# Optimization experiments

Measured on AMD Instinct MI355X. Metric: run time of the kernel, lower is better.

## Reference

```python
import jax, jax.numpy as jnp
import numpy as np

WS = 7  # local window size
NH = 12  # num heads


def _ln(x, g, b, eps=1e-5):
    m = x.mean(-1, keepdims=True)
    v = ((x - m) ** 2).mean(-1, keepdims=True)
    return (x - m) / jnp.sqrt(v + eps) * g + b


def setup_inputs() -> dict:
    key = jax.random.key(0)
    ks = jax.random.split(key, 10)
    B, C, H, W = 8, 384, 112, 112
    r = 4
    s = lambda k, sh: jax.random.normal(k, sh, jnp.float32) * 0.02
    return {
        "x": jax.random.normal(ks[0], (B, C, H, W), jnp.float32),
        "w_qkv": s(ks[1], (3 * C, C)),
        "b_qkv": s(ks[2], (3 * C,)),
        "w_o": s(ks[3], (C, C)),
        "b_o": s(ks[4], (C,)),
        "w_c1": s(ks[5], (C // r, C)),
        "b_c1": s(ks[6], (C // r,)),
        "w_c2": s(ks[7], (C, C // r)),
        "b_c2": s(ks[8], (C,)),
        "g1": jnp.ones((C,), jnp.float32),
        "be1": jnp.zeros((C,), jnp.float32),
        "g2": jnp.ones((C,), jnp.float32),
        "be2": jnp.zeros((C,), jnp.float32),
    }


def reference(x, w_qkv, b_qkv, w_o, b_o, w_c1, b_c1, w_c2, b_c2, g1, be1, g2, be2):
    B, C, H, W = x.shape
    hd = C // NH
    Hw, Ww = H // WS, W // WS
    # window partition: [B,C,H,W] -> [B*Hw*Ww, WS*WS, C]
    win = x.reshape(B, C, Hw, WS, Ww, WS).transpose(0, 2, 4, 1, 3, 5)
    win = win.reshape(-1, C, WS * WS).transpose(0, 2, 1)
    Bn, T, _ = win.shape
    # torch MultiheadAttention: packed in_proj, scaled dot-product, out_proj
    qkv = win @ w_qkv.T + b_qkv
    q, k, v = jnp.split(qkv, 3, axis=-1)
    q = q.reshape(Bn, T, NH, hd)
    k = k.reshape(Bn, T, NH, hd)
    v = v.reshape(Bn, T, NH, hd)
    scores = jnp.einsum('bqhd,bkhd->bhqk', q, k) / jnp.sqrt(jnp.float32(hd))
    a = jax.nn.softmax(scores, axis=-1)
    o = jnp.einsum('bhqk,bkhd->bqhd', a, v).reshape(Bn, T, C)
    o = o @ w_o.T + b_o
    # window reverse: [Bn, WS*WS, C] -> [B,C,H,W]
    attn_out = o.reshape(B, Hw, Ww, WS, WS, C).transpose(0, 5, 1, 3, 2, 4).reshape(B, C, H, W)
    x = x + attn_out
    x = _ln(x.transpose(0, 2, 3, 1), g1, be1).transpose(0, 3, 1, 2)
    # 1x1 conv -> Mish -> 1x1 conv
    h = jnp.einsum('bchw,oc->bohw', x, w_c1) + b_c1[None, :, None, None]
    h = h * jnp.tanh(jax.nn.softplus(h))
    h = jnp.einsum('bchw,oc->bohw', h, w_c2) + b_c2[None, :, None, None]
    x = x + h
    x = _ln(x.transpose(0, 2, 3, 1), g2, be2).transpose(0, 3, 1, 2)
    return x
```

## Files before the change

kernel.cpp:

```cpp
#include <hip/hip_runtime.h>

typedef unsigned short u16;
typedef unsigned int u32;
typedef __bf16 bf16x8 __attribute__((ext_vector_type(8)));
typedef float f32x4 __attribute__((ext_vector_type(4)));

#define NPIX 100352
#define CDIM 384

static __device__ __forceinline__ u16 f2bf(float f) {
  union { float f; u32 u; } un; un.f = f;
  u32 u = un.u;
  return (u16)((u + 0x7fffu + ((u >> 16) & 1u)) >> 16);
}

static __device__ __forceinline__ f32x4 mfma_bf16(bf16x8 a, bf16x8 b, f32x4 c) {
  return __builtin_amdgcn_mfma_f32_16x16x32_bf16(a, b, c, 0, 0, 0);
}

__global__ __launch_bounds__(256) void k_pad_bf16(const float* __restrict__ src,
                                                  u16* __restrict__ dst,
                                                  int R, int Csrc, int Rp, int Cp) {
  int idx = blockIdx.x * 256 + threadIdx.x;
  if (idx >= Rp * Cp) return;
  int r = idx / Cp, c = idx - r * Cp;
  float v = (r < R && c < Csrc) ? src[r * Csrc + c] : 0.f;
  dst[idx] = f2bf(v);
}

__global__ __launch_bounds__(256) void k_gather(const float* __restrict__ x,
                                                float* __restrict__ xw_f32,
                                                u16* __restrict__ xw_bf16) {
  int bid = blockIdx.x;
  int cg = bid % 6;
  int tmp = bid / 6;
  int hh = tmp % 112;
  int b = tmp / 112;
  __shared__ float tile[64][113];
  int tid = threadIdx.x;
  const float* src = x + (((size_t)b * 384 + cg * 64) * 112 + hh) * 112;
  for (int idx = tid; idx < 64 * 112; idx += 256) {
    int c = idx / 112, w = idx - c * 112;
    tile[c][w] = src[(size_t)c * 12544 + w];
  }
  __syncthreads();
  int wh = hh / 7, i = hh - wh * 7;
  for (int idx = tid; idx < 64 * 112; idx += 256) {
    int w = idx >> 6, c = idx & 63;
    int ww = w / 7, j = w - ww * 7;
    size_t t = (((size_t)b * 16 + wh) * 16 + ww) * 49 + i * 7 + j;
    float v = tile[c][w];
    size_t o = t * 384 + cg * 64 + c;
    xw_f32[o] = v;
    xw_bf16[o] = f2bf(v);
  }
}

__global__ __launch_bounds__(256) void k_scatter(const float* __restrict__ t_in,
                                                 float* __restrict__ out) {
  int bid = blockIdx.x;
  int cg = bid % 6;
  int tmp = bid / 6;
  int hh = tmp % 112;
  int b = tmp / 112;
  __shared__ float tile[64][113];
  int tid = threadIdx.x;
  int wh = hh / 7, i = hh - wh * 7;
  for (int idx = tid; idx < 64 * 112; idx += 256) {
    int w = idx >> 6, c = idx & 63;
    int ww = w / 7, j = w - ww * 7;
    size_t t = (((size_t)b * 16 + wh) * 16 + ww) * 49 + i * 7 + j;
    tile[c][w] = t_in[t * 384 + cg * 64 + c];
  }
  __syncthreads();
  float* dst = out + (((size_t)b * 384 + cg * 64) * 112 + hh) * 112;
  for (int idx = tid; idx < 64 * 112; idx += 256) {
    int c = idx / 112, w = idx - c * 112;
    dst[(size_t)c * 12544 + w] = tile[c][w];
  }
}

template <int OUT_BF16, int MISH>
__global__ __launch_bounds__(256) void k_gemm(const u16* __restrict__ A,
                                              const u16* __restrict__ B,
                                              const float* __restrict__ bias, int bias_n,
                                              void* __restrict__ C, int K, int ldc) {
  __shared__ u16 lA[128 * 64];
  __shared__ u16 lB[128 * 64];
  int tid = threadIdx.x;
  int m0 = blockIdx.x * 128;
  int n0 = blockIdx.y * 128;
  int wave = tid >> 6, lane = tid & 63;
  int wr = wave >> 1, wc = wave & 1;
  int lr = lane & 15, lk = (lane >> 4) << 3;
  f32x4 acc[4][4] = {};
  int kt_n = K >> 6;
  for (int kt = 0; kt < kt_n; ++kt) {
    int k0 = kt << 6;
#pragma unroll
    for (int i = 0; i < 4; ++i) {
      int chunk = i * 256 + tid;
      int row = chunk >> 3, c8 = (chunk & 7) << 3;
      *(uint4*)(&lA[(row << 6) + c8]) = *(const uint4*)(A + (size_t)(m0 + row) * K + k0 + c8);
      *(uint4*)(&lB[(row << 6) + c8]) = *(const uint4*)(B + (size_t)(n0 + row) * K + k0 + c8);
    }
    __syncthreads();
#pragma unroll
    for (int ks = 0; ks < 2; ++ks) {
      bf16x8 af[4], bf[4];
#pragma unroll
      for (int f = 0; f < 4; ++f) {
        af[f] = *(const bf16x8*)(&lA[((wr * 64 + f * 16 + lr) << 6) + ks * 32 + lk]);
        bf[f] = *(const bf16x8*)(&lB[((wc * 64 + f * 16 + lr) << 6) + ks * 32 + lk]);
      }
#pragma unroll
      for (int fm = 0; fm < 4; ++fm)
#pragma unroll
        for (int fn = 0; fn < 4; ++fn)
          acc[fm][fn] = mfma_bf16(af[fm], bf[fn], acc[fm][fn]);
    }
    __syncthreads();
  }
  int lg = lane >> 4;
#pragma unroll
  for (int fm = 0; fm < 4; ++fm)
#pragma unroll
    for (int fn = 0; fn < 4; ++fn) {
      int col = n0 + wc * 64 + fn * 16 + lr;
      float bi = (col < bias_n) ? bias[col] : 0.f;
#pragma unroll
      for (int r = 0; r < 4; ++r) {
        int row = m0 + wr * 64 + fm * 16 + lg * 4 + r;
        float v = acc[fm][fn][r] + bi;
        if (MISH) {
          float sp = (v > 20.f) ? v : log1pf(__expf(v));
          v = v * tanhf(sp);
        }
        if (OUT_BF16)
          ((u16*)C)[(size_t)row * ldc + col] = f2bf(v);
        else
          ((float*)C)[(size_t)row * ldc + col] = v;
      }
    }
}

__global__ __launch_bounds__(256) void k_attn(const u16* __restrict__ qkv,
                                              u16* __restrict__ o) {
  __shared__ u16 VT[4][32 * 64];
  __shared__ u16 P[4][64 * 64];
  int tid = threadIdx.x, wave = tid >> 6, lane = tid & 63;
  int gid = blockIdx.x * 4 + wave;
  int win = gid / 12, head = gid - win * 12;
  size_t tb = (size_t)win * 49;
  const u16* q_base = qkv + tb * 1152 + head * 32;
  const u16* k_base = q_base + 384;
  const u16* v_base = q_base + 768;
  u16* vt = VT[wave];
  u16* pp = P[wave];
  int lr = lane & 15, lg = lane >> 4, lk = lg << 3;

  {
    int tok = lane;
    if (tok < 49) {
      const u32* vr = (const u32*)(v_base + (size_t)tok * 1152);
#pragma unroll
      for (int q8 = 0; q8 < 4; ++q8) {
        uint4 a = *(const uint4*)(vr + q8 * 4);
        u32 arr[4] = {a.x, a.y, a.z, a.w};
#pragma unroll
        for (int p = 0; p < 4; ++p) {
          int d = q8 * 8 + p * 2;
          vt[d * 64 + tok] = (u16)(arr[p] & 0xffffu);
          vt[(d + 1) * 64 + tok] = (u16)(arr[p] >> 16);
        }
      }
    } else {
#pragma unroll
      for (int d = 0; d < 32; ++d) vt[d * 64 + tok] = 0;
    }
  }

  f32x4 sc[4][4] = {};
  {
    bf16x8 qf[4], kf[4];
#pragma unroll
    for (int f = 0; f < 4; ++f) {
      int tq = f * 16 + lr; if (tq > 48) tq = 48;
      qf[f] = *(const bf16x8*)(q_base + (size_t)tq * 1152 + lk);
      kf[f] = *(const bf16x8*)(k_base + (size_t)tq * 1152 + lk);
    }
#pragma unroll
    for (int fm = 0; fm < 4; ++fm)
#pragma unroll
      for (int fn = 0; fn < 4; ++fn)
        sc[fm][fn] = mfma_bf16(qf[fm], kf[fn], sc[fm][fn]);
  }

  const float scale = 0.17677669529663687f;
  float denom[4][4];
#pragma unroll
  for (int fm = 0; fm < 4; ++fm)
#pragma unroll
    for (int r = 0; r < 4; ++r) {
      float mx = -1e30f;
#pragma unroll
      for (int fn = 0; fn < 4; ++fn) {
        int col = fn * 16 + lr;
        float s = sc[fm][fn][r] * scale;
        if (col >= 49) s = -1e30f;
        sc[fm][fn][r] = s;
        mx = fmaxf(mx, s);
      }
      for (int off = 8; off; off >>= 1) mx = fmaxf(mx, __shfl_xor(mx, off));
      float sum = 0.f;
#pragma unroll
      for (int fn = 0; fn < 4; ++fn) {
        float e = __expf(sc[fm][fn][r] - mx);
        sc[fm][fn][r] = e;
        sum += e;
      }
      for (int off = 8; off; off >>= 1) sum += __shfl_xor(sum, off);
      denom[fm][r] = sum;
    }

#pragma unroll
  for (int fm = 0; fm < 4; ++fm)
#pragma unroll
    for (int fn = 0; fn < 4; ++fn) {
      int col = fn * 16 + lr;
#pragma unroll
      for (int r = 0; r < 4; ++r) {
        int row = fm * 16 + lg * 4 + r;
        pp[row * 64 + col] = f2bf(sc[fm][fn][r]);
      }
    }
  __syncthreads();

  f32x4 oa[4][2] = {};
#pragma unroll
  for (int ks = 0; ks < 2; ++ks) {
    bf16x8 pf[4], vf[2];
#pragma unroll
    for (int f = 0; f < 4; ++f)
      pf[f] = *(const bf16x8*)(&pp[(f * 16 + lr) * 64 + ks * 32 + lk]);
#pragma unroll
    for (int f = 0; f < 2; ++f)
      vf[f] = *(const bf16x8*)(&vt[(f * 16 + lr) * 64 + ks * 32 + lk]);
#pragma unroll
    for (int fm = 0; fm < 4; ++fm)
#pragma unroll
      for (int fn = 0; fn < 2; ++fn)
        oa[fm][fn] = mfma_bf16(pf[fm], vf[fn], oa[fm][fn]);
  }

#pragma unroll
  for (int fm = 0; fm < 4; ++fm)
#pragma unroll
    for (int fn = 0; fn < 2; ++fn)
#pragma unroll
      for (int r = 0; r < 4; ++r) {
        int q = fm * 16 + lg * 4 + r;
        if (q < 49) {
          float v = oa[fm][fn][r] / denom[fm][r];
          int d = fn * 16 + lr;
          o[(tb + q) * 384 + head * 32 + d] = f2bf(v);
        }
      }
}

template <int WRITE_BF16>
__global__ __launch_bounds__(256) void k_ln(const float* __restrict__ a,
                                            const float* __restrict__ bres,
                                            const float* __restrict__ g,
                                            const float* __restrict__ be,
                                            float* __restrict__ yf,
                                            u16* __restrict__ yb) {
  int wave = threadIdx.x >> 6, lane = threadIdx.x & 63;
  size_t t = (size_t)blockIdx.x * 4 + wave;
  const float* ar = a + t * 384;
  const float* br = bres + t * 384;
  float v[6];
  float s = 0.f, s2 = 0.f;
#pragma unroll
  for (int p = 0; p < 3; ++p) {
    int idx = p * 128 + lane * 2;
    float2 x1 = *(const float2*)(ar + idx);
    float2 x2 = *(const float2*)(br + idx);
    float a0 = x1.x + x2.x, a1 = x1.y + x2.y;
    v[p * 2] = a0; v[p * 2 + 1] = a1;
    s += a0 + a1; s2 += a0 * a0 + a1 * a1;
  }
  for (int off = 32; off; off >>= 1) {
    s += __shfl_xor(s, off);
    s2 += __shfl_xor(s2, off);
  }
  float mean = s * (1.f / 384.f);
  float var = s2 * (1.f / 384.f) - mean * mean;
  float rs = rsqrtf(var + 1e-5f);
  float* yr = yf + t * 384;
#pragma unroll
  for (int p = 0; p < 3; ++p) {
    int idx = p * 128 + lane * 2;
    float2 gg = *(const float2*)(g + idx);
    float2 bb = *(const float2*)(be + idx);
    float y0 = (v[p * 2] - mean) * rs * gg.x + bb.x;
    float y1 = (v[p * 2 + 1] - mean) * rs * gg.y + bb.y;
    *(float2*)(yr + idx) = make_float2(y0, y1);
    if (WRITE_BF16) {
      u32 pk = (u32)f2bf(y0) | ((u32)f2bf(y1) << 16);
      *(u32*)(yb + t * 384 + idx) = pk;
    }
  }
}

extern "C" void kernel_launch(void* const* d_in, const int* in_sizes, int n_in,
                              void* d_out, int out_size, void* d_ws, size_t ws_size,
                              hipStream_t stream) {
  const float* x     = (const float*)d_in[0];
  const float* w_qkv = (const float*)d_in[1];
  const float* b_qkv = (const float*)d_in[2];
  const float* w_o   = (const float*)d_in[3];
  const float* b_o   = (const float*)d_in[4];
  const float* w_c1  = (const float*)d_in[5];
  const float* b_c1  = (const float*)d_in[6];
  const float* w_c2  = (const float*)d_in[7];
  const float* b_c2  = (const float*)d_in[8];
  const float* g1    = (const float*)d_in[9];
  const float* be1   = (const float*)d_in[10];
  const float* g2    = (const float*)d_in[11];
  const float* be2   = (const float*)d_in[12];

  char* ws = (char*)d_ws;
  float* xw_f32 = (float*)ws;
  u16* xw_bf16 = (u16*)(ws + 154140672);
  char* reg3 = ws + 231211008;
  u16* qkv = (u16*)reg3;
  float* attn = (float*)reg3;
  u16* h1 = (u16*)reg3;
  float* hbuf = (float*)(reg3 + 25690112);
  u16* wq_b  = (u16*)(ws + 462422016);
  u16* wo_b  = (u16*)(ws + 463306752);
  u16* wc1_b = (u16*)(ws + 463601664);
  u16* wc2_b = (u16*)(ws + 463699968);
  u16* o_b = xw_bf16;
  u16* y_b = xw_bf16;

  k_pad_bf16<<<1728, 256, 0, stream>>>(w_qkv, wq_b, 1152, 384, 1152, 384);
  k_pad_bf16<<<576, 256, 0, stream>>>(w_o, wo_b, 384, 384, 384, 384);
  k_pad_bf16<<<192, 256, 0, stream>>>(w_c1, wc1_b, 96, 384, 128, 384);
  k_pad_bf16<<<192, 256, 0, stream>>>(w_c2, wc2_b, 384, 96, 384, 128);

  k_gather<<<5376, 256, 0, stream>>>(x, xw_f32, xw_bf16);

  k_gemm<1, 0><<<dim3(784, 9), 256, 0, stream>>>(xw_bf16, wq_b, b_qkv, 1152, (void*)qkv, 384, 1152);

  k_attn<<<6144, 256, 0, stream>>>(qkv, o_b);

  k_gemm<0, 0><<<dim3(784, 3), 256, 0, stream>>>(o_b, wo_b, b_o, 384, (void*)attn, 384, 384);

  k_ln<1><<<25088, 256, 0, stream>>>(xw_f32, attn, g1, be1, xw_f32, y_b);

  k_gemm<1, 1><<<dim3(784, 1), 256, 0, stream>>>(y_b, wc1_b, b_c1, 96, (void*)h1, 384, 128);

  k_gemm<0, 0><<<dim3(784, 3), 256, 0, stream>>>(h1, wc2_b, b_c2, 384, (void*)hbuf, 128, 384);

  k_ln<0><<<25088, 256, 0, stream>>>(xw_f32, hbuf, g2, be2, xw_f32, (u16*)nullptr);

  k_scatter<<<5376, 256, 0, stream>>>(xw_f32, (float*)d_out);
}
```

Measured before the change: 1.096 ms.

## Use direct global-to-LDS loads with XOR swizzle and XCD-aware tile remap in GEMM

The GEMM tile loads now go straight from global memory into LDS through global_load_lds, so the data no longer passes through registers, and the LDS layout uses an XOR swizzle to avoid bank conflicts on fragment reads. Workgroup IDs are remapped so that consecutive tiles land on the same XCD, and the grid axes are swapped so the N tiles of one M row share cached A data. The swizzle has to be consistent between the write and read sides. Synchronisation is unchanged, with no double buffering.

```diff
diff --git a/kernel.cpp b/kernel.cpp
--- a/kernel.cpp
+++ b/kernel.cpp
@@ -16,6 +16,11 @@
 
 static __device__ __forceinline__ f32x4 mfma_bf16(bf16x8 a, bf16x8 b, f32x4 c) {
   return __builtin_amdgcn_mfma_f32_16x16x32_bf16(a, b, c, 0, 0, 0);
+}
+
+static __device__ __forceinline__ void gload_lds16(const u16* g, u16* l) {
+  __builtin_amdgcn_global_load_lds((const __attribute__((address_space(1))) void*)g,
+                                   (__attribute__((address_space(3))) void*)l, 16, 0, 0);
 }
 
 __global__ __launch_bounds__(256) void k_pad_bf16(const float* __restrict__ src,
@@ -88,30 +93,39 @@
   __shared__ u16 lA[128 * 64];
   __shared__ u16 lB[128 * 64];
   int tid = threadIdx.x;
-  int m0 = blockIdx.x * 128;
-  int n0 = blockIdx.y * 128;
+  int nbn = gridDim.x;
+  int nwg = nbn * gridDim.y;
+  int id = blockIdx.y * nbn + blockIdx.x;
+  int q = nwg >> 3;
+  int id2 = (id & 7) * q + (id >> 3);
+  int n0 = (id2 % nbn) * 128;
+  int m0 = (id2 / nbn) * 128;
   int wave = tid >> 6, lane = tid & 63;
   int wr = wave >> 1, wc = wave & 1;
-  int lr = lane & 15, lk = (lane >> 4) << 3;
+  int lr = lane & 15, lg = lane >> 4;
+  int lrow = lane >> 3, lchunk = lane & 7;
+  int csw = (lchunk ^ lrow) << 3;
+  int rsw = lr & 7;
   f32x4 acc[4][4] = {};
   int kt_n = K >> 6;
   for (int kt = 0; kt < kt_n; ++kt) {
     int k0 = kt << 6;
 #pragma unroll
     for (int i = 0; i < 4; ++i) {
-      int chunk = i * 256 + tid;
-      int row = chunk >> 3, c8 = (chunk & 7) << 3;
-      *(uint4*)(&lA[(row << 6) + c8]) = *(const uint4*)(A + (size_t)(m0 + row) * K + k0 + c8);
-      *(uint4*)(&lB[(row << 6) + c8]) = *(const uint4*)(B + (size_t)(n0 + row) * K + k0 + c8);
+      int r0 = i * 32 + wave * 8;
+      int row = r0 + lrow;
+      gload_lds16(A + (size_t)(m0 + row) * K + k0 + csw, &lA[r0 << 6]);
+      gload_lds16(B + (size_t)(n0 + row) * K + k0 + csw, &lB[r0 << 6]);
     }
     __syncthreads();
 #pragma unroll
     for (int ks = 0; ks < 2; ++ks) {
+      int coff = (((ks << 2) + lg) ^ rsw) << 3;
       bf16x8 af[4], bf[4];
 #pragma unroll
       for (int f = 0; f < 4; ++f) {
-        af[f] = *(const bf16x8*)(&lA[((wr * 64 + f * 16 + lr) << 6) + ks * 32 + lk]);
-        bf[f] = *(const bf16x8*)(&lB[((wc * 64 + f * 16 + lr) << 6) + ks * 32 + lk]);
+        af[f] = *(const bf16x8*)(&lA[((wr * 64 + f * 16 + lr) << 6) + coff]);
+        bf[f] = *(const bf16x8*)(&lB[((wc * 64 + f * 16 + lr) << 6) + coff]);
       }
 #pragma unroll
       for (int fm = 0; fm < 4; ++fm)
@@ -121,7 +135,6 @@
     }
     __syncthreads();
   }
-  int lg = lane >> 4;
 #pragma unroll
   for (int fm = 0; fm < 4; ++fm)
 #pragma unroll
@@ -352,17 +365,17 @@
 
   k_gather<<<5376, 256, 0, stream>>>(x, xw_f32, xw_bf16);
 
-  k_gemm<1, 0><<<dim3(784, 9), 256, 0, stream>>>(xw_bf16, wq_b, b_qkv, 1152, (void*)qkv, 384, 1152);
+  k_gemm<1, 0><<<dim3(9, 784), 256, 0, stream>>>(xw_bf16, wq_b, b_qkv, 1152, (void*)qkv, 384, 1152);
 
   k_attn<<<6144, 256, 0, stream>>>(qkv, o_b);
 
-  k_gemm<0, 0><<<dim3(784, 3), 256, 0, stream>>>(o_b, wo_b, b_o, 384, (void*)attn, 384, 384);
+  k_gemm<0, 0><<<dim3(3, 784), 256, 0, stream>>>(o_b, wo_b, b_o, 384, (void*)attn, 384, 384);
 
   k_ln<1><<<25088, 256, 0, stream>>>(xw_f32, attn, g1, be1, xw_f32, y_b);
 
-  k_gemm<1, 1><<<dim3(784, 1), 256, 0, stream>>>(y_b, wc1_b, b_c1, 96, (void*)h1, 384, 128);
-
-  k_gemm<0, 0><<<dim3(784, 3), 256, 0, stream>>>(h1, wc2_b, b_c2, 384, (void*)hbuf, 128, 384);
+  k_gemm<1, 1><<<dim3(1, 784), 256, 0, stream>>>(y_b, wc1_b, b_c1, 96, (void*)h1, 384, 128);
+
+  k_gemm<0, 0><<<dim3(3, 784), 256, 0, stream>>>(h1, wc2_b, b_c2, 384, (void*)hbuf, 128, 384);
 
   k_ln<0><<<25088, 256, 0, stream>>>(xw_f32, hbuf, g2, be2, xw_f32, (u16*)nullptr);
 
```

New measurement: 1.060 ms. 3.3% less time.
